# Optimization experiments

Measured on AMD Instinct MI355X. Metric: run time of the kernel, lower is better.

Reference implementation:

```python
import jax, jax.numpy as jnp
import numpy as np

NUM_HEADS = 16

def rotate_half(x):
    x1, x2 = jnp.split(x, 2, axis=-1)
    return jnp.concatenate((-x2, x1), axis=-1)

def setup_inputs() -> dict:
    key = jax.random.key(0)
    ks = jax.random.split(key, 5)
    b, n, dim, hd = 2, 2048, 1024, 64
    return {
        "x": jax.random.normal(ks[0], (b, n, dim), dtype=jnp.float32),
        "Wqkv": jax.random.normal(ks[1], (3 * dim, dim), dtype=jnp.float32) * (dim ** -0.5),
        "Wproj": jax.random.normal(ks[2], (dim, dim), dtype=jnp.float32) * (dim ** -0.5),
        "bproj": jnp.zeros((dim,), dtype=jnp.float32),
        "sin": jax.random.normal(ks[3], (n, hd), dtype=jnp.float32),
        "cos": jax.random.normal(ks[4], (n, hd), dtype=jnp.float32),
    }

def reference(x, Wqkv, Wproj, bproj, sin, cos):
    b, n, dim = x.shape
    h = NUM_HEADS
    d = dim // h
    qkv = x @ Wqkv.T
    qkv = qkv.reshape(b, n, 3, h, d).transpose(2, 0, 3, 1, 4)
    q, k, v = qkv[0], qkv[1], qkv[2]
    # RoPE: sin/cos [n, d] broadcast over [b, h, n, d]
    q = q * cos + rotate_half(q) * sin
    k = k * cos + rotate_half(k) * sin
    # SDPA (non-causal, no dropout at eval)
    scale = d ** -0.5
    scores = jnp.einsum("bhnd,bhmd->bhnm", q, k) * scale
    attn = jax.nn.softmax(scores, axis=-1)
    out = jnp.einsum("bhnm,bhmd->bhnd", attn, v)
    # merge heads: [b, h, n, d] -> [b, n, h*d]
    out = out.transpose(0, 2, 1, 3).reshape(b, n, dim)
    return out @ Wproj.T + bproj
```

## Files before the change

### kernel.cpp

```cpp
#include <hip/hip_runtime.h>
#include <hip/hip_fp16.h>

typedef _Float16 f16;
typedef _Float16 half8 __attribute__((ext_vector_type(8)));
typedef _Float16 half4v __attribute__((ext_vector_type(4)));
typedef float f32x4 __attribute__((ext_vector_type(4)));

#define QSCALE 0.18033688011112042f
#define SHIFT2 17.312340490667560f

__device__ __forceinline__ void gload_lds16(const void* g, void* lds) {
  __builtin_amdgcn_global_load_lds(
      (__attribute__((address_space(1))) void*)g,
      (__attribute__((address_space(3))) void*)lds, 16, 0, 0);
}

__global__ __launch_bounds__(256) void cvt_all_kernel(
    const float* __restrict__ x, const float* __restrict__ wqkv,
    const float* __restrict__ wproj, f16* __restrict__ xh,
    f16* __restrict__ wqkvh, f16* __restrict__ wprojh) {
  int i = blockIdx.x * 256 + threadIdx.x;
  const float* src; f16* dst; int off;
  if (i < 1048576)      { src = x;     dst = xh;     off = i; }
  else if (i < 1835008) { src = wqkv;  dst = wqkvh;  off = i - 1048576; }
  else                  { src = wproj; dst = wprojh; off = i - 1835008; }
  float4 v = ((const float4*)src)[off];
  half4v o;
  o.x = (f16)v.x; o.y = (f16)v.y; o.z = (f16)v.z; o.w = (f16)v.w;
  ((half4v*)dst)[off] = o;
}

template<int EPI>
__global__ __launch_bounds__(256) void hgemm_kernel(
    const f16* __restrict__ A16, const f16* __restrict__ B, int K,
    const float* __restrict__ cosT, const float* __restrict__ sinT,
    f16* __restrict__ Qout, f16* __restrict__ Kout, f16* __restrict__ Vtout,
    const float* __restrict__ bias, float* __restrict__ Cout) {
  constexpr int BN = (EPI == 0) ? 128 : 64;
  constexpr int NJ = (EPI == 0) ? 4 : 2;
  __shared__ f16 As[2][128 * 32];
  __shared__ f16 Bs[2][BN * 32];
  const int tid = threadIdx.x;
  const int lane = tid & 63, w = tid >> 6;
  const int fr = lane & 15, fkg = lane >> 4;
  const int wm = (w >> 1) * 64;
  const int wn = (EPI == 0) ? (w & 1) * 64 : (w & 1) * 16;
  const long long rowBase = (long long)blockIdx.x * 128;
  const long long colBase = (long long)blockIdx.y * BN;

  f32x4 acc[4][NJ] = {};
  const f16* Ab = A16 + rowBase * K;
  const f16* Bb = B + colBase * K;

  const int srow = lane >> 2;
  const int kcol = ((lane & 3) ^ ((lane >> 3) & 3)) * 8;
  const int sw = (fkg ^ ((fr >> 1) & 3)) * 8;

  auto stage = [&](int buf, int k0) {
#pragma unroll
    for (int r = 0; r < 2; ++r) {
      int c = r * 4 + w;
      gload_lds16(Ab + (long long)(c * 16 + srow) * K + k0 + kcol, &As[buf][c * 512]);
    }
    if (EPI == 0) {
#pragma unroll
      for (int r = 0; r < 2; ++r) {
        int c = r * 4 + w;
        gload_lds16(Bb + (long long)(c * 16 + srow) * K + k0 + kcol, &Bs[buf][c * 512]);
      }
    } else {
      int c = w;
      gload_lds16(Bb + (long long)(c * 16 + srow) * K + k0 + kcol, &Bs[buf][c * 512]);
    }
  };

  const int NT = K >> 5;
  stage(0, 0);
  stage(1, 32);
  for (int t = 0; t < NT; ++t) {
    const int buf = t & 1;
    const int k0 = t << 5;
    if (t + 1 < NT) {
      if constexpr (EPI == 0) asm volatile("s_waitcnt vmcnt(4)" ::: "memory");
      else                    asm volatile("s_waitcnt vmcnt(3)" ::: "memory");
    } else {
      asm volatile("s_waitcnt vmcnt(0)" ::: "memory");
    }
    __builtin_amdgcn_s_barrier();
    __builtin_amdgcn_sched_barrier(0);
    half8 a[4], b[NJ];
#pragma unroll
    for (int i = 0; i < 4; ++i)
      a[i] = *(const half8*)(&As[buf][((wm >> 4) + i) * 512 + fr * 32 + sw]);
#pragma unroll
    for (int j = 0; j < NJ; ++j) {
      int chunk = (EPI == 0) ? ((wn >> 4) + j) : ((wn >> 4) + j * 2);
      b[j] = *(const half8*)(&Bs[buf][chunk * 512 + fr * 32 + sw]);
    }
    asm volatile("s_waitcnt lgkmcnt(0)" ::: "memory");
    __builtin_amdgcn_sched_barrier(0);
    __builtin_amdgcn_s_barrier();
    if (t + 2 < NT) stage(buf, k0 + 64);
#pragma unroll
    for (int i = 0; i < 4; ++i)
#pragma unroll
      for (int j = 0; j < NJ; ++j)
        acc[i][j] = __builtin_amdgcn_mfma_f32_16x16x32_f16(a[i], b[j], acc[i][j], 0, 0, 0);
  }

  if (EPI == 0) {
#pragma unroll
    for (int i = 0; i < 4; ++i) {
#pragma unroll
      for (int r = 0; r < 4; ++r) {
        int rg = (int)rowBase + wm + i * 16 + fkg * 4 + r;
        int bidx = rg >> 11, nn = rg & 2047;
#pragma unroll
        for (int j = 0; j < 4; ++j) {
          int cg = (int)colBase + wn + j * 16 + fr;
          int t = cg >> 10, cc = cg & 1023;
          int head = cc >> 6, d = cc & 63;
          int bh = bidx * 16 + head;
          float v = acc[i][j][r];
          if (t == 2) {
            Vtout[((long long)bh * 64 + d) * 2048 + nn] = (f16)v;
          } else {
            float pal = acc[i][j ^ 2][r];
            float cs = cosT[nn * 64 + d];
            float sn = sinT[nn * 64 + d];
            v = v * cs + (d < 32 ? -pal : pal) * sn;
            if (t == 0) v *= QSCALE;
            f16 hv = (f16)v;
            if (t == 0) Qout[((long long)bh * 2048 + nn) * 64 + d] = hv;
            else        Kout[((long long)bh * 2048 + nn) * 64 + d] = hv;
          }
        }
      }
    }
  } else {
#pragma unroll
    for (int i = 0; i < 4; ++i)
#pragma unroll
      for (int r = 0; r < 4; ++r) {
        long long rg = rowBase + wm + i * 16 + fkg * 4 + r;
#pragma unroll
        for (int j = 0; j < NJ; ++j) {
          int cg = (int)colBase + wn + j * 32 + fr;
          Cout[rg * 1024 + cg] = acc[i][j][r] + bias[cg];
        }
      }
  }
}

__global__ __launch_bounds__(256) void attn_kernel(
    const f16* __restrict__ Q, const f16* __restrict__ Kb,
    const f16* __restrict__ Vt, f16* __restrict__ Om) {
  __shared__ f16 Ks[64 * 72];
  __shared__ f16 Vs[64 * 72];
  __shared__ f16 Ps[4][32 * 72];
  const int tid = threadIdx.x;
  const int lane = tid & 63, w = tid >> 6;
  const int fr = lane & 15, fkg = lane >> 4, fk = fkg * 8;
  const int bh = blockIdx.y;
  const int q0 = blockIdx.x * 128 + w * 32;
  f16* Psw = &Ps[w][0];

  half8 aq[2][2];
#pragma unroll
  for (int m = 0; m < 2; ++m)
#pragma unroll
    for (int ks = 0; ks < 2; ++ks)
      aq[m][ks] = *(const half8*)(Q + ((long long)bh * 2048 + q0 + m * 16 + fr) * 64 +
                                  ks * 32 + fk);

  half8 ones_frag;
#pragma unroll
  for (int j = 0; j < 8; ++j) ones_frag[j] = (fr == 0) ? (f16)1.0f : (f16)0.0f;

  f32x4 acc[2][5] = {};

  const int soff = tid * 8;
  const int skr0 = soff >> 6, sd0 = soff & 63;
  half8 kreg[2], vreg[2];
#pragma unroll
  for (int c = 0; c < 2; ++c) {
    int kr = skr0 + c * 32;
    kreg[c] = *(const half8*)(Kb + ((long long)bh * 2048 + kr) * 64 + sd0);
    vreg[c] = *(const half8*)(Vt + ((long long)bh * 64 + kr) * 2048 + sd0);
  }

  for (int kv0 = 0; kv0 < 2048; kv0 += 64) {
    __syncthreads();
#pragma unroll
    for (int c = 0; c < 2; ++c) {
      int kr = skr0 + c * 32;
      *(half8*)(Ks + kr * 72 + sd0) = kreg[c];
      *(half8*)(Vs + kr * 72 + sd0) = vreg[c];
    }
    if (kv0 + 64 < 2048) {
#pragma unroll
      for (int c = 0; c < 2; ++c) {
        int kr = skr0 + c * 32;
        kreg[c] = *(const half8*)(Kb + ((long long)bh * 2048 + kv0 + 64 + kr) * 64 + sd0);
        vreg[c] = *(const half8*)(Vt + ((long long)bh * 64 + kr) * 2048 + kv0 + 64 + sd0);
      }
    }
    __syncthreads();

    f32x4 z[2][4];
#pragma unroll
    for (int n = 0; n < 4; ++n) {
      half8 bk0 = *(const half8*)(Ks + (n * 16 + fr) * 72 + fk);
      half8 bk1 = *(const half8*)(Ks + (n * 16 + fr) * 72 + 32 + fk);
#pragma unroll
      for (int m = 0; m < 2; ++m) {
        f32x4 t = {0.f, 0.f, 0.f, 0.f};
        t = __builtin_amdgcn_mfma_f32_16x16x32_f16(bk0, aq[m][0], t, 0, 0, 0);
        t = __builtin_amdgcn_mfma_f32_16x16x32_f16(bk1, aq[m][1], t, 0, 0, 0);
        z[m][n] = t;
      }
    }

#pragma unroll
    for (int m = 0; m < 2; ++m)
#pragma unroll
      for (int n = 0; n < 4; ++n) {
        half4v h;
#pragma unroll
        for (int r = 0; r < 4; ++r)
          h[r] = (f16)__builtin_amdgcn_exp2f(z[m][n][r] - SHIFT2);
        *(half4v*)(Psw + (m * 16 + fr) * 72 + n * 16 + fkg * 4) = h;
      }

#pragma unroll
    for (int ks = 0; ks < 2; ++ks) {
      half8 ap[2];
#pragma unroll
      for (int m = 0; m < 2; ++m) {
        ap[m] = *(const half8*)(Psw + (m * 16 + fr) * 72 + ks * 32 + fk);
        acc[m][4] = __builtin_amdgcn_mfma_f32_16x16x32_f16(ap[m], ones_frag, acc[m][4], 0, 0, 0);
      }
#pragma unroll
      for (int dd = 0; dd < 4; ++dd) {
        half8 bv = *(const half8*)(Vs + (dd * 16 + fr) * 72 + ks * 32 + fk);
#pragma unroll
        for (int m = 0; m < 2; ++m)
          acc[m][dd] = __builtin_amdgcn_mfma_f32_16x16x32_f16(ap[m], bv, acc[m][dd], 0, 0, 0);
      }
    }
  }

  const int b = bh >> 4, h = bh & 15;
#pragma unroll
  for (int m = 0; m < 2; ++m)
#pragma unroll
    for (int r = 0; r < 4; ++r) {
      int nn = q0 + m * 16 + fkg * 4 + r;
      float l = __shfl(acc[m][4][r], lane & 48);
      float inv = 1.f / l;
#pragma unroll
      for (int dd = 0; dd < 4; ++dd)
        Om[((long long)b * 2048 + nn) * 1024 + h * 64 + dd * 16 + fr] =
            (f16)(acc[m][dd][r] * inv);
    }
}

extern "C" void kernel_launch(void* const* d_in, const int* in_sizes, int n_in,
                              void* d_out, int out_size, void* d_ws, size_t ws_size,
                              hipStream_t stream) {
  (void)in_sizes; (void)n_in; (void)out_size; (void)ws_size;
  const float* x     = (const float*)d_in[0];
  const float* Wqkv  = (const float*)d_in[1];
  const float* Wproj = (const float*)d_in[2];
  const float* bproj = (const float*)d_in[3];
  const float* sinT  = (const float*)d_in[4];
  const float* cosT  = (const float*)d_in[5];
  float* out = (float*)d_out;

  f16* ws     = (f16*)d_ws;
  f16* xh     = ws;
  f16* Om     = ws;
  f16* Wqkvh  = ws + 4194304;
  f16* Wprojh = ws + 7340032;
  f16* Qb     = ws + 8388608;
  f16* Kb     = ws + 12582912;
  f16* Vtb    = ws + 16777216;

  cvt_all_kernel<<<8192, 256, 0, stream>>>(x, Wqkv, Wproj, xh, Wqkvh, Wprojh);

  hgemm_kernel<0><<<dim3(32, 24), 256, 0, stream>>>(
      xh, Wqkvh, 1024, cosT, sinT, Qb, Kb, Vtb, nullptr, nullptr);

  attn_kernel<<<dim3(16, 32), 256, 0, stream>>>(Qb, Kb, Vtb, Om);

  hgemm_kernel<1><<<dim3(32, 16), 256, 0, stream>>>(
      Om, Wprojh, 1024, nullptr, nullptr, nullptr, nullptr, nullptr, bproj, out);
}
```

Before: 126.1 us.

## Double-buffer K/V via direct global-to-LDS loads with swizzled layout in attention

Replaces the register-staged single K/V LDS buffer in the attention kernel with double-buffered tiles filled by direct global-to-LDS loads, so the next tile's fetch overlaps compute. It uses an XOR-swizzled unpadded layout to avoid bank conflicts. It also swaps the MFMA operand order so outputs can be stored as 4-wide vectors, and remaps blocks to a 1D grid that spreads heads across XCDs for L2 locality. Hand-placed waitcnt and barriers add fragility if the vmcnt counts do not match the number of issued loads.

```diff
diff --git a/kernel.cpp b/kernel.cpp
--- a/kernel.cpp
+++ b/kernel.cpp
@@ -155,15 +155,21 @@
 __global__ __launch_bounds__(256) void attn_kernel(
     const f16* __restrict__ Q, const f16* __restrict__ Kb,
     const f16* __restrict__ Vt, f16* __restrict__ Om) {
-  __shared__ f16 Ks[64 * 72];
-  __shared__ f16 Vs[64 * 72];
+  __shared__ f16 Ks[2][64 * 64];
+  __shared__ f16 Vs[2][64 * 64];
   __shared__ f16 Ps[4][32 * 72];
   const int tid = threadIdx.x;
   const int lane = tid & 63, w = tid >> 6;
   const int fr = lane & 15, fkg = lane >> 4, fk = fkg * 8;
-  const int bh = blockIdx.y;
-  const int q0 = blockIdx.x * 128 + w * 32;
+
+  const int lin = blockIdx.x;
+  const int slot = lin >> 3;
+  const int bh = (lin & 7) * 4 + (slot >> 4);
+  const int q0 = (slot & 15) * 128 + w * 32;
   f16* Psw = &Ps[w][0];
+
+  const f16* Kbh = Kb + (long long)bh * 2048 * 64;
+  const f16* Vbh = Vt + (long long)bh * 64 * 2048;
 
   half8 aq[2][2];
 #pragma unroll
@@ -177,47 +183,43 @@
 #pragma unroll
   for (int j = 0; j < 8; ++j) ones_frag[j] = (fr == 0) ? (f16)1.0f : (f16)0.0f;
 
-  f32x4 acc[2][5] = {};
-
-  const int soff = tid * 8;
-  const int skr0 = soff >> 6, sd0 = soff & 63;
-  half8 kreg[2], vreg[2];
-#pragma unroll
-  for (int c = 0; c < 2; ++c) {
-    int kr = skr0 + c * 32;
-    kreg[c] = *(const half8*)(Kb + ((long long)bh * 2048 + kr) * 64 + sd0);
-    vreg[c] = *(const half8*)(Vt + ((long long)bh * 64 + kr) * 2048 + sd0);
-  }
-
-  for (int kv0 = 0; kv0 < 2048; kv0 += 64) {
-    __syncthreads();
+  f32x4 acc[2][4] = {};
+  f32x4 accL[2] = {};
+
+  const int srow = lane >> 3;
+  const int ssub = ((lane & 7) ^ (lane >> 3)) * 8;
+
+  auto stage = [&](int buf, int kv0) {
 #pragma unroll
     for (int c = 0; c < 2; ++c) {
-      int kr = skr0 + c * 32;
-      *(half8*)(Ks + kr * 72 + sd0) = kreg[c];
-      *(half8*)(Vs + kr * 72 + sd0) = vreg[c];
-    }
-    if (kv0 + 64 < 2048) {
-#pragma unroll
-      for (int c = 0; c < 2; ++c) {
-        int kr = skr0 + c * 32;
-        kreg[c] = *(const half8*)(Kb + ((long long)bh * 2048 + kv0 + 64 + kr) * 64 + sd0);
-        vreg[c] = *(const half8*)(Vt + ((long long)bh * 64 + kr) * 2048 + kv0 + 64 + sd0);
-      }
-    }
-    __syncthreads();
+      int rb = w * 16 + c * 8;
+      gload_lds16(Kbh + (long long)(kv0 + rb + srow) * 64 + ssub,
+                  &Ks[buf][rb * 64]);
+      gload_lds16(Vbh + (long long)(rb + srow) * 2048 + kv0 + ssub,
+                  &Vs[buf][rb * 64]);
+    }
+  };
+
+  stage(0, 0);
+  stage(1, 64);
+  for (int t = 0; t < 32; ++t) {
+    const int buf = t & 1;
+    if (t + 1 < 32) asm volatile("s_waitcnt vmcnt(4)" ::: "memory");
+    else            asm volatile("s_waitcnt vmcnt(0)" ::: "memory");
+    __builtin_amdgcn_s_barrier();
+    __builtin_amdgcn_sched_barrier(0);
 
     f32x4 z[2][4];
 #pragma unroll
     for (int n = 0; n < 4; ++n) {
-      half8 bk0 = *(const half8*)(Ks + (n * 16 + fr) * 72 + fk);
-      half8 bk1 = *(const half8*)(Ks + (n * 16 + fr) * 72 + 32 + fk);
+      half8 bk0 = *(const half8*)(&Ks[buf][(n * 16 + fr) * 64 + ((fkg ^ (fr & 7)) * 8)]);
+      half8 bk1 = *(const half8*)(&Ks[buf][(n * 16 + fr) * 64 + (((4 | fkg) ^ (fr & 7)) * 8)]);
 #pragma unroll
       for (int m = 0; m < 2; ++m) {
-        f32x4 t = {0.f, 0.f, 0.f, 0.f};
-        t = __builtin_amdgcn_mfma_f32_16x16x32_f16(bk0, aq[m][0], t, 0, 0, 0);
-        t = __builtin_amdgcn_mfma_f32_16x16x32_f16(bk1, aq[m][1], t, 0, 0, 0);
-        z[m][n] = t;
+        f32x4 tz = {0.f, 0.f, 0.f, 0.f};
+        tz = __builtin_amdgcn_mfma_f32_16x16x32_f16(bk0, aq[m][0], tz, 0, 0, 0);
+        tz = __builtin_amdgcn_mfma_f32_16x16x32_f16(bk1, aq[m][1], tz, 0, 0, 0);
+        z[m][n] = tz;
       }
     }
 
@@ -238,31 +240,38 @@
 #pragma unroll
       for (int m = 0; m < 2; ++m) {
         ap[m] = *(const half8*)(Psw + (m * 16 + fr) * 72 + ks * 32 + fk);
-        acc[m][4] = __builtin_amdgcn_mfma_f32_16x16x32_f16(ap[m], ones_frag, acc[m][4], 0, 0, 0);
+        accL[m] = __builtin_amdgcn_mfma_f32_16x16x32_f16(ones_frag, ap[m], accL[m], 0, 0, 0);
       }
 #pragma unroll
       for (int dd = 0; dd < 4; ++dd) {
-        half8 bv = *(const half8*)(Vs + (dd * 16 + fr) * 72 + ks * 32 + fk);
+        half8 av = *(const half8*)(&Vs[buf][(dd * 16 + fr) * 64 +
+                                            ((((ks << 2) | fkg) ^ (fr & 7)) * 8)]);
 #pragma unroll
         for (int m = 0; m < 2; ++m)
-          acc[m][dd] = __builtin_amdgcn_mfma_f32_16x16x32_f16(ap[m], bv, acc[m][dd], 0, 0, 0);
-      }
-    }
+          acc[m][dd] = __builtin_amdgcn_mfma_f32_16x16x32_f16(av, ap[m], acc[m][dd], 0, 0, 0);
+      }
+    }
+
+    asm volatile("s_waitcnt lgkmcnt(0)" ::: "memory");
+    __builtin_amdgcn_sched_barrier(0);
+    __builtin_amdgcn_s_barrier();
+    if (t + 2 < 32) stage(buf, (t + 2) * 64);
   }
 
   const int b = bh >> 4, h = bh & 15;
 #pragma unroll
-  for (int m = 0; m < 2; ++m)
-#pragma unroll
-    for (int r = 0; r < 4; ++r) {
-      int nn = q0 + m * 16 + fkg * 4 + r;
-      float l = __shfl(acc[m][4][r], lane & 48);
-      float inv = 1.f / l;
-#pragma unroll
-      for (int dd = 0; dd < 4; ++dd)
-        Om[((long long)b * 2048 + nn) * 1024 + h * 64 + dd * 16 + fr] =
-            (f16)(acc[m][dd][r] * inv);
-    }
+  for (int m = 0; m < 2; ++m) {
+    float l = __shfl(accL[m][0], fr);
+    float inv = 1.f / l;
+#pragma unroll
+    for (int dd = 0; dd < 4; ++dd) {
+      half4v o;
+#pragma unroll
+      for (int r = 0; r < 4; ++r) o[r] = (f16)(acc[m][dd][r] * inv);
+      *(half4v*)(&Om[((long long)b * 2048 + q0 + m * 16 + fr) * 1024 +
+                     h * 64 + dd * 16 + fkg * 4]) = o;
+    }
+  }
 }
 
 extern "C" void kernel_launch(void* const* d_in, const int* in_sizes, int n_in,
@@ -291,7 +300,7 @@
   hgemm_kernel<0><<<dim3(32, 24), 256, 0, stream>>>(
       xh, Wqkvh, 1024, cosT, sinT, Qb, Kb, Vtb, nullptr, nullptr);
 
-  attn_kernel<<<dim3(16, 32), 256, 0, stream>>>(Qb, Kb, Vtb, Om);
+  attn_kernel<<<512, 256, 0, stream>>>(Qb, Kb, Vtb, Om);
 
   hgemm_kernel<1><<<dim3(32, 16), 256, 0, stream>>>(
       Om, Wprojh, 1024, nullptr, nullptr, nullptr, nullptr, nullptr, bproj, out);
```

Result: slower. 130.6 us (+3.6%).
